# Kernel tuning notes

Hardware: AMD Instinct MI355X
Metric: run time of the kernel (lower is better)

The kernel has to match this reference:

```python
import jax, jax.numpy as jnp
import numpy as np

VAR = 1.0
BETA = 500.0
ALPHA = 1.0


def setup_inputs() -> dict:
    key = jax.random.key(0)
    k1, k2, k3 = jax.random.split(key, 3)
    N, D = 8192, 64
    y_true = jax.random.normal(k1, (N, D), dtype=jnp.float32)
    y_pred = jax.random.normal(k2, (N, D), dtype=jnp.float32)
    encoded = jax.random.normal(k3, (N, D), dtype=jnp.float32)
    return {"y_true": y_true, "y_pred": y_pred, "encoded": encoded}


def reference(y_true, y_pred, encoded):
    # --- entropy rate term (KDE-based) ---
    n_batch = encoded.shape[0]
    # pairwise squared euclidean distances, [N, N]
    sq = jnp.sum(encoded * encoded, axis=-1)  # [N]
    d2 = sq[:, None] + sq[None, :] - 2.0 * (encoded @ encoded.T)
    d2 = jnp.maximum(d2, 0.0)
    kde_contribution = jnp.mean(jax.nn.logsumexp(-0.5 * d2 / VAR, axis=1))
    c = jnp.log(jnp.float32(n_batch))
    IXT = (c - kde_contribution) / jnp.log(jnp.float32(2.0))  # nats -> bits

    # --- distortion term (MSE, mean reduction) ---
    distortion = jnp.mean((y_pred - y_true) ** 2)

    loss = ALPHA * IXT + BETA * distortion
    return (loss, IXT, distortion)
```

## Files before the change

### kernel.cpp

```cpp
#include <hip/hip_runtime.h>
#include <math.h>

#define NROWS 8192
#define DDIM  64
#define JSPLIT 32
#define JSPAN  (NROWS / JSPLIT)
#define LOG2E  1.4426950408889634f
#define SKIP_THR (-28.0f)
#define APAD  72

typedef __bf16 bf16x8 __attribute__((ext_vector_type(8)));
typedef float  f32x4  __attribute__((ext_vector_type(4)));


__global__ __launch_bounds__(256)
void prep_kernel(const float* __restrict__ yt, const float* __restrict__ yp,
                 const float* __restrict__ enc,
                 __bf16* __restrict__ ebf, __bf16* __restrict__ ebl,
                 float* __restrict__ hp2, float* __restrict__ mse_part,
                 float* __restrict__ sum_s) {
    int bid = blockIdx.x;
    int t   = threadIdx.x;
    if (bid < 256) {
        int off = bid * 2048 + t * 8;
        const float4* e4 = (const float4*)(enc + off);
        float4 x = e4[0], y = e4[1];
        bf16x8 v, w;
        v[0]=(__bf16)x.x; v[1]=(__bf16)x.y; v[2]=(__bf16)x.z; v[3]=(__bf16)x.w;
        v[4]=(__bf16)y.x; v[5]=(__bf16)y.y; v[6]=(__bf16)y.z; v[7]=(__bf16)y.w;
        w[0]=(__bf16)(x.x*LOG2E); w[1]=(__bf16)(x.y*LOG2E);
        w[2]=(__bf16)(x.z*LOG2E); w[3]=(__bf16)(x.w*LOG2E);
        w[4]=(__bf16)(y.x*LOG2E); w[5]=(__bf16)(y.y*LOG2E);
        w[6]=(__bf16)(y.z*LOG2E); w[7]=(__bf16)(y.w*LOG2E);
        *(bf16x8*)(ebf + off) = v;
        *(bf16x8*)(ebl + off) = w;
    } else if (bid < 768) {
        int idx = (bid - 256) * 256 + t;
        const float4* t4 = (const float4*)yt;
        const float4* p4 = (const float4*)yp;
        float4 a = t4[idx], b = p4[idx];
        float dx=b.x-a.x, dy=b.y-a.y, dz=b.z-a.z, dw=b.w-a.w;
        float s = dx*dx + dy*dy + dz*dz + dw*dw;
        #pragma unroll
        for (int off = 32; off > 0; off >>= 1) s += __shfl_down(s, off, 64);
        __shared__ float ls[4];
        int lane = t & 63, w = t >> 6;
        if (lane == 0) ls[w] = s;
        __syncthreads();
        if (t == 0) mse_part[bid - 256] = ls[0] + ls[1] + ls[2] + ls[3];
    } else if (bid < 896) {
        int wv = t >> 6, ln = t & 63;
        int tile = (bid - 768) * 4 + wv;
        int lm = ln & 15, lk = ln >> 4;
        const float* r = enc + (tile * 16 + lm) * DDIM;
        bf16x8 f0, f1, g0, g1;
        {
            const float4* q = (const float4*)(r + lk * 8);
            float4 x = q[0], y = q[1];
            f0[0]=(__bf16)x.x; f0[1]=(__bf16)x.y; f0[2]=(__bf16)x.z; f0[3]=(__bf16)x.w;
            f0[4]=(__bf16)y.x; f0[5]=(__bf16)y.y; f0[6]=(__bf16)y.z; f0[7]=(__bf16)y.w;
            g0[0]=(__bf16)(x.x*LOG2E); g0[1]=(__bf16)(x.y*LOG2E);
            g0[2]=(__bf16)(x.z*LOG2E); g0[3]=(__bf16)(x.w*LOG2E);
            g0[4]=(__bf16)(y.x*LOG2E); g0[5]=(__bf16)(y.y*LOG2E);
            g0[6]=(__bf16)(y.z*LOG2E); g0[7]=(__bf16)(y.w*LOG2E);
        }
        {
            const float4* q = (const float4*)(r + 32 + lk * 8);
            float4 x = q[0], y = q[1];
            f1[0]=(__bf16)x.x; f1[1]=(__bf16)x.y; f1[2]=(__bf16)x.z; f1[3]=(__bf16)x.w;
            f1[4]=(__bf16)y.x; f1[5]=(__bf16)y.y; f1[6]=(__bf16)y.z; f1[7]=(__bf16)y.w;
            g1[0]=(__bf16)(x.x*LOG2E); g1[1]=(__bf16)(x.y*LOG2E);
            g1[2]=(__bf16)(x.z*LOG2E); g1[3]=(__bf16)(x.w*LOG2E);
            g1[4]=(__bf16)(y.x*LOG2E); g1[5]=(__bf16)(y.y*LOG2E);
            g1[6]=(__bf16)(y.z*LOG2E); g1[7]=(__bf16)(y.w*LOG2E);
        }
        f32x4 acc = {0.f, 0.f, 0.f, 0.f};
        acc = __builtin_amdgcn_mfma_f32_16x16x32_bf16(f0, g0, acc, 0, 0, 0);
        acc = __builtin_amdgcn_mfma_f32_16x16x32_bf16(f1, g1, acc, 0, 0, 0);
        #pragma unroll
        for (int reg = 0; reg < 4; ++reg) {
            int rc = lk * 4 + reg;
            if (lm == rc) hp2[tile * 16 + rc] = 0.5f * acc[reg];
        }
    } else {
        int off = (bid - 896) * 2048 + t * 8;
        float4 z = make_float4(0.f, 0.f, 0.f, 0.f);
        ((float4*)(sum_s + off))[0] = z;
        ((float4*)(sum_s + off))[1] = z;
    }
}

__global__ __launch_bounds__(256)
__attribute__((amdgpu_waves_per_eu(4, 8)))
void pairwise_kernel(const __bf16* __restrict__ ebf, const __bf16* __restrict__ ebl,
                     const float* __restrict__ hp2, float* __restrict__ sum_s) {
    __shared__ __bf16 alds[256 * APAD];
    __shared__ float  hlds[256];

    int t  = threadIdx.x;
    int wv = t >> 6, ln = t & 63;
    int lm = ln & 15, lk = ln >> 4;
    int I0B = blockIdx.x * 256;
    int j0  = blockIdx.y * JSPAN;

    {
        const bf16x8* src = (const bf16x8*)(ebf + (I0B + t) * DDIM);
        bf16x8* dst = (bf16x8*)(alds + t * APAD);
        #pragma unroll
        for (int k = 0; k < 8; ++k) dst[k] = src[k];
        hlds[t] = hp2[I0B + t];
    }
    __syncthreads();

    float eacc[16];
    #pragma unroll
    for (int i = 0; i < 16; ++i) eacc[i] = 0.f;

    for (int js = 0; js < JSPAN; js += 32) {
        int Jt = j0 + js;
        const __bf16* rp = ebl + (Jt + lm) * DDIM + lk * 8;
        const __bf16* rq = ebl + (Jt + 16 + lm) * DDIM + lk * 8;
        bf16x8 b0 = *(const bf16x8*)(rp);
        bf16x8 b1 = *(const bf16x8*)(rp + 32);
        bf16x8 c0 = *(const bf16x8*)(rq);
        bf16x8 c1 = *(const bf16x8*)(rq + 32);
        float  nhj = -hp2[Jt + lm];
        float  nhk = -hp2[Jt + 16 + lm];

        #pragma unroll
        for (int mt = 0; mt < 4; ++mt) {
            int arow = wv * 64 + mt * 16 + lm;
            const bf16x8* ap = (const bf16x8*)(alds + arow * APAD);
            bf16x8 a0 = ap[lk];
            bf16x8 a1 = ap[4 + lk];
            const f32x4 hv = *(const f32x4*)(hlds + wv * 64 + mt * 16 + lk * 4);

            f32x4 acc1 = {nhj - hv[0], nhj - hv[1], nhj - hv[2], nhj - hv[3]};
            acc1 = __builtin_amdgcn_mfma_f32_16x16x32_bf16(a0, b0, acc1, 0, 0, 0);
            acc1 = __builtin_amdgcn_mfma_f32_16x16x32_bf16(a1, b1, acc1, 0, 0, 0);
            f32x4 acc2 = {nhk - hv[0], nhk - hv[1], nhk - hv[2], nhk - hv[3]};
            acc2 = __builtin_amdgcn_mfma_f32_16x16x32_bf16(a0, c0, acc2, 0, 0, 0);
            acc2 = __builtin_amdgcn_mfma_f32_16x16x32_bf16(a1, c1, acc2, 0, 0, 0);

            float m1 = fmaxf(fmaxf(acc1[0], acc1[1]), fmaxf(acc1[2], acc1[3]));
            if (__any(m1 > SKIP_THR)) {
                #pragma unroll
                for (int reg = 0; reg < 4; ++reg)
                    eacc[mt * 4 + reg] += __builtin_amdgcn_exp2f(acc1[reg]);
            }
            float m2 = fmaxf(fmaxf(acc2[0], acc2[1]), fmaxf(acc2[2], acc2[3]));
            if (__any(m2 > SKIP_THR)) {
                #pragma unroll
                for (int reg = 0; reg < 4; ++reg)
                    eacc[mt * 4 + reg] += __builtin_amdgcn_exp2f(acc2[reg]);
            }
        }
    }
    #pragma unroll
    for (int i = 0; i < 16; ++i) {
        float v = eacc[i];
        v += __shfl_xor(v, 1, 64);
        v += __shfl_xor(v, 2, 64);
        v += __shfl_xor(v, 4, 64);
        v += __shfl_xor(v, 8, 64);
        if (lm == 0) {
            int mt = i >> 2, reg = i & 3;
            atomicAdd(&sum_s[I0B + wv * 64 + mt * 16 + lk * 4 + reg], v);
        }
    }
}

__global__ __launch_bounds__(1024)
void finalize_kernel(const float* __restrict__ sum_s,
                     const float* __restrict__ mse_part,
                     float* __restrict__ out) {
    int t = threadIdx.x, lane = t & 63, w = t >> 6;
    float s = 0.0f;
    #pragma unroll
    for (int u = 0; u < 8; ++u) s += __logf(sum_s[t * 8 + u]);
    float m = (t < 512) ? mse_part[t] : 0.f;
    #pragma unroll
    for (int off = 32; off > 0; off >>= 1) {
        s += __shfl_down(s, off, 64);
        m += __shfl_down(m, off, 64);
    }
    __shared__ float rs[16], rm[16];
    if (lane == 0) { rs[w] = s; rm[w] = m; }
    __syncthreads();
    if (t == 0) {
        float tot = 0.f, mtot = 0.f;
        #pragma unroll
        for (int i = 0; i < 16; ++i) { tot += rs[i]; mtot += rm[i]; }
        float kde = tot / (float)NROWS;
        float c   = logf((float)NROWS);
        float IXT = (c - kde) / logf(2.0f);
        float mse = mtot / (float)(NROWS * DDIM);
        out[0] = 1.0f * IXT + 500.0f * mse;
        out[1] = IXT;
        out[2] = mse;
    }
}

extern "C" void kernel_launch(void* const* d_in, const int* in_sizes, int n_in,
                              void* d_out, int out_size, void* d_ws, size_t ws_size,
                              hipStream_t stream) {
    const float* y_true  = (const float*)d_in[0];
    const float* y_pred  = (const float*)d_in[1];
    const float* encoded = (const float*)d_in[2];
    float* out = (float*)d_out;

    float*  wsf      = (float*)d_ws;
    float*  mse_part = wsf;
    float*  sum_s    = wsf + 512;
    float*  hp2      = wsf + 512 + NROWS;
    __bf16* ebf      = (__bf16*)(wsf + 512 + 2 * NROWS);
    __bf16* ebl      = ebf + NROWS * DDIM;

    prep_kernel<<<900, 256, 0, stream>>>(y_true, y_pred, encoded,
                                         ebf, ebl, hp2, mse_part, sum_s);
    pairwise_kernel<<<dim3(NROWS / 256, JSPLIT), 256, 0, stream>>>(ebf, ebl, hp2, sum_s);
    finalize_kernel<<<1, 1024, 0, stream>>>(sum_s, mse_part, out);
}
```

Baseline: 86.61 us.

## Fuse finalize into pairwise kernel via last-block counter and prefetch B tiles

Removes the separate finalize kernel launch. An atomic done counter elects the last pairwise block, which reads the accumulated sums with atomic loads and writes the final loss. It also software-prefetches the next J-tile's B operands and norms into registers before the current tile's MFMAs, to hide global load latency. The cost is extra registers and an atomic epilogue in every block.

```diff
diff --git a/kernel.cpp b/kernel.cpp
--- a/kernel.cpp
+++ b/kernel.cpp
@@ -8,6 +8,7 @@
 #define LOG2E  1.4426950408889634f
 #define SKIP_THR (-28.0f)
 #define APAD  72
+#define NBLK 1024
 
 typedef __bf16 bf16x8 __attribute__((ext_vector_type(8)));
 typedef float  f32x4  __attribute__((ext_vector_type(4)));
@@ -18,7 +19,7 @@
                  const float* __restrict__ enc,
                  __bf16* __restrict__ ebf, __bf16* __restrict__ ebl,
                  float* __restrict__ hp2, float* __restrict__ mse_part,
-                 float* __restrict__ sum_s) {
+                 float* __restrict__ sum_s, int* __restrict__ done) {
     int bid = blockIdx.x;
     int t   = threadIdx.x;
     if (bid < 256) {
@@ -87,13 +88,48 @@
         float4 z = make_float4(0.f, 0.f, 0.f, 0.f);
         ((float4*)(sum_s + off))[0] = z;
         ((float4*)(sum_s + off))[1] = z;
+        if (bid == 896 && t == 0) *done = 0;
+    }
+}
+
+__device__ __attribute__((noinline))
+void finalize_tail(float* __restrict__ sum_s, const float* __restrict__ mse_part,
+                   float* __restrict__ out, int t) {
+    float s = 0.0f;
+    #pragma unroll
+    for (int u = 0; u < 32; ++u) {
+        float v = atomicAdd(&sum_s[t * 32 + u], 0.0f);
+        s += __logf(v);
+    }
+    float m = mse_part[t] + mse_part[t + 256];
+    #pragma unroll
+    for (int off = 32; off > 0; off >>= 1) {
+        s += __shfl_down(s, off, 64);
+        m += __shfl_down(m, off, 64);
+    }
+    __shared__ float rs[4], rm[4];
+    int lane = t & 63, w = t >> 6;
+    if (lane == 0) { rs[w] = s; rm[w] = m; }
+    __syncthreads();
+    if (t == 0) {
+        float tot  = rs[0] + rs[1] + rs[2] + rs[3];
+        float mtot = rm[0] + rm[1] + rm[2] + rm[3];
+        float kde = tot / (float)NROWS;
+        float c   = logf((float)NROWS);
+        float IXT = (c - kde) / logf(2.0f);
+        float mse = mtot / (float)(NROWS * DDIM);
+        out[0] = 1.0f * IXT + 500.0f * mse;
+        out[1] = IXT;
+        out[2] = mse;
     }
 }
 
 __global__ __launch_bounds__(256)
 __attribute__((amdgpu_waves_per_eu(4, 8)))
 void pairwise_kernel(const __bf16* __restrict__ ebf, const __bf16* __restrict__ ebl,
-                     const float* __restrict__ hp2, float* __restrict__ sum_s) {
+                     const float* __restrict__ hp2, float* __restrict__ sum_s,
+                     const float* __restrict__ mse_part, int* __restrict__ done,
+                     float* __restrict__ out) {
     __shared__ __bf16 alds[256 * APAD];
     __shared__ float  hlds[256];
 
@@ -116,16 +152,25 @@
     #pragma unroll
     for (int i = 0; i < 16; ++i) eacc[i] = 0.f;
 
+    const __bf16* rp = ebl + (j0 + lm) * DDIM + lk * 8;
+    const __bf16* rq = ebl + (j0 + 16 + lm) * DDIM + lk * 8;
+    bf16x8 b0 = *(const bf16x8*)(rp);
+    bf16x8 b1 = *(const bf16x8*)(rp + 32);
+    bf16x8 c0 = *(const bf16x8*)(rq);
+    bf16x8 c1 = *(const bf16x8*)(rq + 32);
+    float  nhj = -hp2[j0 + lm];
+    float  nhk = -hp2[j0 + 16 + lm];
+
     for (int js = 0; js < JSPAN; js += 32) {
-        int Jt = j0 + js;
-        const __bf16* rp = ebl + (Jt + lm) * DDIM + lk * 8;
-        const __bf16* rq = ebl + (Jt + 16 + lm) * DDIM + lk * 8;
-        bf16x8 b0 = *(const bf16x8*)(rp);
-        bf16x8 b1 = *(const bf16x8*)(rp + 32);
-        bf16x8 c0 = *(const bf16x8*)(rq);
-        bf16x8 c1 = *(const bf16x8*)(rq + 32);
-        float  nhj = -hp2[Jt + lm];
-        float  nhk = -hp2[Jt + 16 + lm];
+        int jn = (js + 32 < JSPAN) ? (j0 + js + 32) : j0;
+        const __bf16* rpn = ebl + (jn + lm) * DDIM + lk * 8;
+        const __bf16* rqn = ebl + (jn + 16 + lm) * DDIM + lk * 8;
+        bf16x8 pb0 = *(const bf16x8*)(rpn);
+        bf16x8 pb1 = *(const bf16x8*)(rpn + 32);
+        bf16x8 pc0 = *(const bf16x8*)(rqn);
+        bf16x8 pc1 = *(const bf16x8*)(rqn + 32);
+        float  pnhj = -hp2[jn + lm];
+        float  pnhk = -hp2[jn + 16 + lm];
 
         #pragma unroll
         for (int mt = 0; mt < 4; ++mt) {
@@ -155,6 +200,7 @@
                     eacc[mt * 4 + reg] += __builtin_amdgcn_exp2f(acc2[reg]);
             }
         }
+        b0 = pb0; b1 = pb1; c0 = pc0; c1 = pc1; nhj = pnhj; nhk = pnhk;
     }
     #pragma unroll
     for (int i = 0; i < 16; ++i) {
@@ -168,37 +214,13 @@
             atomicAdd(&sum_s[I0B + wv * 64 + mt * 16 + lk * 4 + reg], v);
         }
     }
-}
-
-__global__ __launch_bounds__(1024)
-void finalize_kernel(const float* __restrict__ sum_s,
-                     const float* __restrict__ mse_part,
-                     float* __restrict__ out) {
-    int t = threadIdx.x, lane = t & 63, w = t >> 6;
-    float s = 0.0f;
-    #pragma unroll
-    for (int u = 0; u < 8; ++u) s += __logf(sum_s[t * 8 + u]);
-    float m = (t < 512) ? mse_part[t] : 0.f;
-    #pragma unroll
-    for (int off = 32; off > 0; off >>= 1) {
-        s += __shfl_down(s, off, 64);
-        m += __shfl_down(m, off, 64);
-    }
-    __shared__ float rs[16], rm[16];
-    if (lane == 0) { rs[w] = s; rm[w] = m; }
+
+    asm volatile("s_waitcnt vmcnt(0)" ::: "memory");
+    __shared__ int lastFlag;
+    if (t == 0) lastFlag = (atomicAdd(done, 1) == NBLK - 1);
     __syncthreads();
-    if (t == 0) {
-        float tot = 0.f, mtot = 0.f;
-        #pragma unroll
-        for (int i = 0; i < 16; ++i) { tot += rs[i]; mtot += rm[i]; }
-        float kde = tot / (float)NROWS;
-        float c   = logf((float)NROWS);
-        float IXT = (c - kde) / logf(2.0f);
-        float mse = mtot / (float)(NROWS * DDIM);
-        out[0] = 1.0f * IXT + 500.0f * mse;
-        out[1] = IXT;
-        out[2] = mse;
-    }
+    if (!lastFlag) return;
+    finalize_tail(sum_s, mse_part, out, t);
 }
 
 extern "C" void kernel_launch(void* const* d_in, const int* in_sizes, int n_in,
@@ -213,11 +235,12 @@
     float*  mse_part = wsf;
     float*  sum_s    = wsf + 512;
     float*  hp2      = wsf + 512 + NROWS;
-    __bf16* ebf      = (__bf16*)(wsf + 512 + 2 * NROWS);
+    int*    done     = (int*)(wsf + 512 + 2 * NROWS);
+    __bf16* ebf      = (__bf16*)(wsf + 512 + 2 * NROWS + 4);
     __bf16* ebl      = ebf + NROWS * DDIM;
 
     prep_kernel<<<900, 256, 0, stream>>>(y_true, y_pred, encoded,
-                                         ebf, ebl, hp2, mse_part, sum_s);
-    pairwise_kernel<<<dim3(NROWS / 256, JSPLIT), 256, 0, stream>>>(ebf, ebl, hp2, sum_s);
-    finalize_kernel<<<1, 1024, 0, stream>>>(sum_s, mse_part, out);
-}
+                                         ebf, ebl, hp2, mse_part, sum_s, done);
+    pairwise_kernel<<<dim3(NROWS / 256, JSPLIT), 256, 0, stream>>>(
+        ebf, ebl, hp2, sum_s, mse_part, done, out);
+}
```

Result: slower. 177.7 us (+105.1%).
